# Kernel optimization log

Measured on AMD Instinct MI355X. Metric: run time of the kernel, lower is better.

## Reference

```python
import jax, jax.numpy as jnp
import numpy as np

BS = 4
EMBED = 256
HEADS = 8
LEVELS = 4
POINTS = 4
HD = EMBED // HEADS  # 32
SHAPES = np.array([[96, 96], [48, 48], [24, 24], [12, 12]], dtype=np.int64)
LQ = int((SHAPES[:, 0] * SHAPES[:, 1]).sum())  # 12240


def _offset_bias():
    # faithful to MSDeformableAttention._reset_parameters grid init
    thetas = np.arange(HEADS, dtype=np.float32) * (2.0 * np.pi / HEADS)
    g = np.stack([np.cos(thetas), np.sin(thetas)], -1)
    g = g / np.abs(g).max(-1, keepdims=True)
    g = np.tile(g.reshape(HEADS, 1, 1, 2), (1, LEVELS, POINTS, 1))
    g = g * np.arange(1, POINTS + 1, dtype=np.float32).reshape(1, 1, -1, 1)
    return jnp.asarray(g.reshape(-1), dtype=jnp.float32)


def setup_inputs() -> dict:
    key = jax.random.key(0)
    ks = jax.random.split(key, 8)
    tp = HEADS * LEVELS * POINTS
    d = {}
    d["query"] = jax.random.normal(ks[0], (BS, LQ, EMBED), jnp.float32)
    d["reference_points"] = jax.random.uniform(ks[1], (BS, LQ, LEVELS, 2), jnp.float32)
    d["value"] = jax.random.normal(ks[2], (BS, LQ, EMBED), jnp.float32)
    d["value_spatial_shapes"] = SHAPES  # static numpy, int
    d["W_off"] = jax.random.normal(ks[3], (EMBED, tp * 2), jnp.float32) * 0.01
    d["b_off"] = _offset_bias()
    d["W_attn"] = jax.random.normal(ks[4], (EMBED, tp), jnp.float32) * 0.02
    d["b_attn"] = jnp.zeros((tp,), jnp.float32)
    d["W_val"] = jax.random.normal(ks[5], (EMBED, EMBED), jnp.float32) * (1.0 / np.sqrt(EMBED).astype(np.float32))
    d["b_val"] = jnp.zeros((EMBED,), jnp.float32)
    d["W_out"] = jax.random.normal(ks[6], (EMBED, EMBED), jnp.float32) * (1.0 / np.sqrt(EMBED).astype(np.float32))
    d["b_out"] = jnp.zeros((EMBED,), jnp.float32)
    return d


def _bilinear_sample(img, grid):
    # img: [B,H,W,C]; grid: [B,Q,P,2] in [-1,1] (x,y)
    # matches F.grid_sample(mode='bilinear', padding_mode='zeros', align_corners=False)
    B, H, W, C = img.shape
    gx = (grid[..., 0] + 1.0) * (W * 0.5) - 0.5
    gy = (grid[..., 1] + 1.0) * (H * 0.5) - 0.5
    x0 = jnp.floor(gx)
    y0 = jnp.floor(gy)
    wx = gx - x0
    wy = gy - y0
    x0i = x0.astype(jnp.int32)
    y0i = y0.astype(jnp.int32)
    x1i = x0i + 1
    y1i = y0i + 1
    flat = img.reshape(B, H * W, C)

    def corner(xi, yi, w):
        valid = (xi >= 0) & (xi < W) & (yi >= 0) & (yi < H)
        idx = jnp.clip(yi, 0, H - 1) * W + jnp.clip(xi, 0, W - 1)
        v = jnp.take_along_axis(flat, idx.reshape(B, -1, 1), axis=1)
        v = v.reshape(idx.shape + (C,))
        return v * (w * valid)[..., None]

    return (corner(x0i, y0i, (1.0 - wx) * (1.0 - wy))
            + corner(x1i, y0i, wx * (1.0 - wy))
            + corner(x0i, y1i, (1.0 - wx) * wy)
            + corner(x1i, y1i, wx * wy))


def reference(query, reference_points, value, value_spatial_shapes,
              W_off, b_off, W_attn, b_attn, W_val, b_val, W_out, b_out):
    shapes = np.asarray(value_spatial_shapes)  # static [L,2] (H,W)
    bs, Lq, _ = query.shape
    v = (value @ W_val + b_val).reshape(bs, -1, HEADS, HD)  # [bs,Lv,H,hd]
    off = (query @ W_off + b_off).reshape(bs, Lq, HEADS, LEVELS, POINTS, 2)
    aw = jax.nn.softmax((query @ W_attn + b_attn).reshape(bs, Lq, HEADS, LEVELS * POINTS), axis=-1)
    aw = aw.reshape(bs, Lq, HEADS, LEVELS, POINTS)
    # normalizer is (W,H) per level
    norm = jnp.asarray(shapes[:, ::-1].copy(), jnp.float32).reshape(1, 1, 1, LEVELS, 1, 2)
    loc = reference_points[:, :, None, :, None, :] + off / norm
    grids = 2.0 * loc - 1.0  # [bs,Lq,H,L,P,2]

    acc = jnp.zeros((bs * HEADS, Lq, HD), query.dtype)
    start = 0
    for lvl in range(LEVELS):
        h, w = int(shapes[lvl, 0]), int(shapes[lvl, 1])
        v_l = v[:, start:start + h * w].reshape(bs, h, w, HEADS, HD)
        v_l = v_l.transpose(0, 3, 1, 2, 4).reshape(bs * HEADS, h, w, HD)
        g_l = grids[:, :, :, lvl].transpose(0, 2, 1, 3, 4).reshape(bs * HEADS, Lq, POINTS, 2)
        s_l = _bilinear_sample(v_l, g_l)  # [bs*H, Lq, P, hd]
        w_l = aw[:, :, :, lvl].transpose(0, 2, 1, 3).reshape(bs * HEADS, Lq, POINTS)
        acc = acc + jnp.einsum('bqpc,bqp->bqc', s_l, w_l)
        start += h * w

    out = acc.reshape(bs, HEADS, Lq, HD).transpose(0, 2, 1, 3).reshape(bs, Lq, EMBED)
    return out @ W_out + b_out
```

## Files before the change

kernel.cpp:

```cpp
#include <hip/hip_runtime.h>
#include <hip/hip_bf16.h>

static constexpr int BS     = 4;
static constexpr int EMBED  = 256;
static constexpr int HEADS  = 8;
static constexpr int LEVELS = 4;
static constexpr int POINTS = 4;
static constexpr int HD     = 32;
static constexpr int LQ     = 12240;
static constexpr int NROW   = BS * LQ;
static constexpr int LVL_W[4]  = {96, 48, 24, 12};
static constexpr int LVL_H[4]  = {96, 48, 24, 12};
static constexpr int LVL_ST[4] = {0, 9216, 11520, 12096};

typedef __attribute__((ext_vector_type(8))) short short8;
typedef __attribute__((ext_vector_type(4))) float f32x4;
typedef __attribute__((ext_vector_type(2))) float f32x2;
typedef _Float16 h2 __attribute__((ext_vector_type(2)));

__device__ __forceinline__ unsigned short f2bf(float f) {
    unsigned int u = __float_as_uint(f);
    unsigned int r = (u + 0x7FFFu + ((u >> 16) & 1u)) >> 16;
    return (unsigned short)r;
}

__device__ __forceinline__ unsigned int pkh(float a, float b) {
    const unsigned int ua = __builtin_bit_cast(unsigned short, (_Float16)a);
    const unsigned int ub = __builtin_bit_cast(unsigned short, (_Float16)b);
    return ua | (ub << 16);
}

__device__ __forceinline__ float dot2(float acc, unsigned int v, unsigned int w) {
#if __has_builtin(__builtin_amdgcn_fdot2)
    return __builtin_amdgcn_fdot2(__builtin_bit_cast(h2, v),
                                  __builtin_bit_cast(h2, w), acc, false);
#else
    asm("v_dot2_f32_f16 %0, %1, %2, %0" : "+v"(acc) : "v"(v), "v"(w));
    return acc;
#endif
}

__global__ __launch_bounds__(256) void prep_weights(
    const float* __restrict__ W_off, const float* __restrict__ W_attn,
    const float* __restrict__ W_val, const float* __restrict__ W_out,
    unsigned short* __restrict__ WT_oa, unsigned short* __restrict__ WT_val,
    unsigned short* __restrict__ WT_out)
{
    const int gid = blockIdx.x * 256 + threadIdx.x;
    const int k = gid & 255;
    const int n = gid >> 8;
    if (n < 384) {
        const float v = (n < 256) ? W_off[k * 256 + n] : W_attn[k * 128 + (n - 256)];
        WT_oa[n * 256 + k] = f2bf(v);
    } else if (n < 640) {
        const int nn = n - 384;
        WT_val[nn * 256 + k] = f2bf(W_val[k * 256 + nn]);
    } else {
        const int nn = n - 640;
        WT_out[nn * 256 + k] = f2bf(W_out[k * 256 + nn]);
    }
}

__global__ __launch_bounds__(256, 5) void gemm_vo(
    const float* __restrict__ Aval, const float* __restrict__ Aqry,
    const unsigned short* __restrict__ Wval, const unsigned short* __restrict__ Woa,
    const float* __restrict__ bval, const float* __restrict__ boff,
    const float* __restrict__ battn,
    unsigned short* __restrict__ Vout, float* __restrict__ OAout)
{
    constexpr int NTW = 2;
    constexpr int NB  = 128;
    constexpr int K   = 256;
    __shared__ __align__(16) unsigned short As[64][40];
    __shared__ __align__(16) unsigned short Bs[NB][40];

    const int x    = blockIdx.x;
    const bool isV = (x < 2);
    const float* A = isV ? Aval : Aqry;
    const unsigned short* Wt = isV ? Wval : Woa;
    const int n0   = isV ? x * 128 : (x - 2) * 128;

    const int tid = threadIdx.x;
    const int m0 = blockIdx.y * 64;
    const int w  = tid >> 6;
    const int l  = tid & 63;
    const int lm = l & 15;
    const int lq = l >> 4;

    const int sr = tid >> 2;
    const int kg = (tid & 3) * 8;

    float4 pa0, pa1;
    short8 pb[NTW];

    auto gload = [&](int k0) {
        const float* ap = &A[(size_t)(m0 + sr) * K + k0 + kg];
        pa0 = *(const float4*)ap;
        pa1 = *(const float4*)(ap + 4);
        #pragma unroll
        for (int i = 0; i < NTW; ++i) {
            const int slot = tid + i * 256;
            const int n  = slot >> 2;
            const int kk = (slot & 3) * 8;
            pb[i] = *(const short8*)&Wt[(size_t)(n0 + n) * K + k0 + kk];
        }
    };

    f32x4 acc[4][NTW];
    #pragma unroll
    for (int rg = 0; rg < 4; ++rg)
        #pragma unroll
        for (int nt = 0; nt < NTW; ++nt)
            acc[rg][nt] = (f32x4){0.f, 0.f, 0.f, 0.f};

    gload(0);
    #pragma unroll 2
    for (int k0 = 0; k0 < K; k0 += 32) {
        uint4 pk;
        pk.x = (unsigned int)f2bf(pa0.x) | ((unsigned int)f2bf(pa0.y) << 16);
        pk.y = (unsigned int)f2bf(pa0.z) | ((unsigned int)f2bf(pa0.w) << 16);
        pk.z = (unsigned int)f2bf(pa1.x) | ((unsigned int)f2bf(pa1.y) << 16);
        pk.w = (unsigned int)f2bf(pa1.z) | ((unsigned int)f2bf(pa1.w) << 16);
        *(uint4*)&As[sr][kg] = pk;
        #pragma unroll
        for (int i = 0; i < NTW; ++i) {
            const int slot = tid + i * 256;
            const int n  = slot >> 2;
            const int kk = (slot & 3) * 8;
            *(short8*)&Bs[n][kk] = pb[i];
        }
        __syncthreads();

        if (k0 + 32 < K) gload(k0 + 32);

        short8 af[4];
        #pragma unroll
        for (int rg = 0; rg < 4; ++rg)
            af[rg] = *(const short8*)&As[rg * 16 + lm][lq * 8];
        #pragma unroll
        for (int nt = 0; nt < NTW; ++nt) {
            const short8 bf = *(const short8*)&Bs[(w * NTW + nt) * 16 + lm][lq * 8];
            #pragma unroll
            for (int rg = 0; rg < 4; ++rg)
                acc[rg][nt] = __builtin_amdgcn_mfma_f32_16x16x32_bf16(af[rg], bf, acc[rg][nt], 0, 0, 0);
        }
        __syncthreads();
    }

    #pragma unroll
    for (int nt = 0; nt < NTW; ++nt) {
        const int col = n0 + (w * NTW + nt) * 16 + lm;
        float b;
        if (isV) b = bval[col];
        else     b = (col < 256) ? boff[col] : battn[col - 256];
        #pragma unroll
        for (int rg = 0; rg < 4; ++rg)
            #pragma unroll
            for (int r = 0; r < 4; ++r) {
                const int row = m0 + rg * 16 + lq * 4 + r;
                const float v = acc[rg][nt][r] + b;
                if (isV) Vout[(size_t)row * 256 + col] =
                             __builtin_bit_cast(unsigned short, (_Float16)v);
                else     OAout[(size_t)row * 384 + col] = v;
            }
    }
}

template <int NTW, bool A_BF16, bool OUT_BF16>
__global__ __launch_bounds__(256, 5) void gemm_mfma(
    const void* __restrict__ Av, const unsigned short* __restrict__ Wt,
    const float* __restrict__ bias0, const float* __restrict__ bias1, int nsplit,
    void* __restrict__ Cv, int N)
{
    constexpr int NB = NTW * 64;
    constexpr int K  = 256;
    __shared__ __align__(16) unsigned short As[64][40];
    __shared__ __align__(16) unsigned short Bs[NB][40];

    const int tid = threadIdx.x;
    const int m0 = blockIdx.y * 64;
    const int n0 = blockIdx.x * NB;
    const int w  = tid >> 6;
    const int l  = tid & 63;
    const int lm = l & 15;
    const int lq = l >> 4;

    const int sr = tid >> 2;
    const int kg = (tid & 3) * 8;

    float4 pa0, pa1; short8 pa_bf;
    short8 pb[NTW];

    auto gload = [&](int k0) {
        if (A_BF16) {
            const unsigned short* A = (const unsigned short*)Av;
            pa_bf = *(const short8*)&A[(size_t)(m0 + sr) * K + k0 + kg];
        } else {
            const float* A = (const float*)Av;
            const float* ap = &A[(size_t)(m0 + sr) * K + k0 + kg];
            pa0 = *(const float4*)ap;
            pa1 = *(const float4*)(ap + 4);
        }
        #pragma unroll
        for (int i = 0; i < NTW; ++i) {
            const int slot = tid + i * 256;
            const int n  = slot >> 2;
            const int kk = (slot & 3) * 8;
            pb[i] = *(const short8*)&Wt[(size_t)(n0 + n) * K + k0 + kk];
        }
    };

    f32x4 acc[4][NTW];
    #pragma unroll
    for (int rg = 0; rg < 4; ++rg)
        #pragma unroll
        for (int nt = 0; nt < NTW; ++nt)
            acc[rg][nt] = (f32x4){0.f, 0.f, 0.f, 0.f};

    gload(0);
    #pragma unroll 2
    for (int k0 = 0; k0 < K; k0 += 32) {
        if (A_BF16) {
            *(short8*)&As[sr][kg] = pa_bf;
        } else {
            uint4 pk;
            pk.x = (unsigned int)f2bf(pa0.x) | ((unsigned int)f2bf(pa0.y) << 16);
            pk.y = (unsigned int)f2bf(pa0.z) | ((unsigned int)f2bf(pa0.w) << 16);
            pk.z = (unsigned int)f2bf(pa1.x) | ((unsigned int)f2bf(pa1.y) << 16);
            pk.w = (unsigned int)f2bf(pa1.z) | ((unsigned int)f2bf(pa1.w) << 16);
            *(uint4*)&As[sr][kg] = pk;
        }
        #pragma unroll
        for (int i = 0; i < NTW; ++i) {
            const int slot = tid + i * 256;
            const int n  = slot >> 2;
            const int kk = (slot & 3) * 8;
            *(short8*)&Bs[n][kk] = pb[i];
        }
        __syncthreads();

        if (k0 + 32 < K) gload(k0 + 32);

        short8 af[4];
        #pragma unroll
        for (int rg = 0; rg < 4; ++rg)
            af[rg] = *(const short8*)&As[rg * 16 + lm][lq * 8];
        #pragma unroll
        for (int nt = 0; nt < NTW; ++nt) {
            const short8 bf = *(const short8*)&Bs[(w * NTW + nt) * 16 + lm][lq * 8];
            #pragma unroll
            for (int rg = 0; rg < 4; ++rg)
                acc[rg][nt] = __builtin_amdgcn_mfma_f32_16x16x32_bf16(af[rg], bf, acc[rg][nt], 0, 0, 0);
        }
        __syncthreads();
    }

    #pragma unroll
    for (int nt = 0; nt < NTW; ++nt) {
        const int col = n0 + (w * NTW + nt) * 16 + lm;
        const float b = (col < nsplit) ? bias0[col] : bias1[col - nsplit];
        #pragma unroll
        for (int rg = 0; rg < 4; ++rg)
            #pragma unroll
            for (int r = 0; r < 4; ++r) {
                const int row = m0 + rg * 16 + lq * 4 + r;
                const float v = acc[rg][nt][r] + b;
                if (OUT_BF16) ((unsigned short*)Cv)[(size_t)row * N + col] = f2bf(v);
                else          ((float*)Cv)[(size_t)row * N + col] = v;
            }
    }
}

__global__ __launch_bounds__(256, 7) void sample_kernel(
    const unsigned short* __restrict__ V,
    const float* __restrict__ OA,
    const float* __restrict__ refp,
    unsigned short* __restrict__ ACC)
{
    __shared__ __align__(16) unsigned int pr_o[512][4];
    __shared__ __align__(16) unsigned int pr_w[512][2];

    const int tid = threadIdx.x;

    const unsigned bx = blockIdx.x;
    const int xcd  = bx & 7;
    const int slot = bx >> 3;
    const int batch = xcd >> 1;
    const int wb   = slot * 2 + (xcd & 1);
    const int row0 = batch * LQ + wb * 4;

    {
        const int g = tid & 31;
        const int r = g >> 3;
        const int h = g & 7;
        const int L = tid >> 5;
        const int prow = row0 + r;
        const float* rowp = OA + (size_t)prow * 384;

        const float lg0 = rowp[256 + h * 16 + L];
        const float lg1 = rowp[256 + h * 16 + L + 8];

        float* smax = (float*)pr_w;
        float* ssum = smax + 264;
        smax[L * 33 + g] = fmaxf(lg0, lg1);
        __syncthreads();
        float m = smax[g];
        #pragma unroll
        for (int k = 1; k < 8; ++k) m = fmaxf(m, smax[k * 33 + g]);
        const float e0 = __expf(lg0 - m);
        const float e1 = __expf(lg1 - m);
        ssum[L * 33 + g] = e0 + e1;
        __syncthreads();
        float sden = ssum[g];
        #pragma unroll
        for (int k = 1; k < 8; ++k) sden += ssum[k * 33 + g];
        const float inv = 1.0f / sden;

        uint2 wstash[2];
        int   sidx[2];
        #pragma unroll
        for (int ss = 0; ss < 2; ++ss) {
            const int lp  = L + ss * 8;
            const int s   = lp * 32 + g;
            const int lvl = lp >> 2;
            const int Wl = LVL_W[lvl], Hl = LVL_H[lvl], st = LVL_ST[lvl];

            const float2 oxy = *(const float2*)&rowp[h * 32 + lp * 2];
            const float2 rxy = *(const float2*)&refp[(size_t)prow * 8 + lvl * 2];
            const float wgt = (ss ? e1 : e0) * inv;

            const float gx = (rxy.x + oxy.x / (float)Wl) * (float)Wl - 0.5f;
            const float gy = (rxy.y + oxy.y / (float)Hl) * (float)Hl - 0.5f;

            const float fx = floorf(gx), fy = floorf(gy);
            const float wx = gx - fx,    wy = gy - fy;
            const int x0 = (int)fx, y0 = (int)fy;
            const int x1 = x0 + 1,  y1 = y0 + 1;

            const bool bx0 = ((unsigned)x0 < (unsigned)Wl);
            const bool bx1 = ((unsigned)x1 < (unsigned)Wl);
            const bool by0 = ((unsigned)y0 < (unsigned)Hl);
            const bool by1 = ((unsigned)y1 < (unsigned)Hl);
            const float w00 = (bx0 && by0) ? (1.f - wx) * (1.f - wy) * wgt : 0.f;
            const float w10 = (bx1 && by0) ? wx * (1.f - wy) * wgt : 0.f;
            const float w01 = (bx0 && by1) ? (1.f - wx) * wy * wgt : 0.f;
            const float w11 = (bx1 && by1) ? wx * wy * wgt : 0.f;

            const int cx0 = min(max(x0, 0), Wl - 1);
            const int cx1 = min(max(x1, 0), Wl - 1);
            const int cy0 = min(max(y0, 0), Hl - 1);
            const int cy1 = min(max(y1, 0), Hl - 1);

            uint4 o;
            o.x = (unsigned int)(st + cy0 * Wl + cx0) * 512u;
            o.y = (unsigned int)(st + cy0 * Wl + cx1) * 512u;
            o.z = (unsigned int)(st + cy1 * Wl + cx0) * 512u;
            o.w = (unsigned int)(st + cy1 * Wl + cx1) * 512u;
            *(uint4*)&pr_o[s][0] = o;

            wstash[ss] = make_uint2(pkh(w00, w10), pkh(w01, w11));
            sidx[ss] = s;
        }
        __syncthreads();
        *(uint2*)&pr_w[sidx[0]][0] = wstash[0];
        *(uint2*)&pr_w[sidx[1]][0] = wstash[1];
    }
    __syncthreads();

    const int w    = tid >> 6;
    const int l    = tid & 63;
    const int half = l >> 5;
    const int head = (l >> 2) & 7;
    const int c16  = (l & 3) * 16;

    const int row  = __builtin_amdgcn_readfirstlane(row0 + w);
    const char* vrow = (const char*)V + (size_t)batch * ((size_t)LQ * 512);
    const unsigned int lane_byte = (unsigned int)(head * 64 + c16);
    const int sid0 = half * 256 + w * 8 + head;

    constexpr unsigned SEL_LO = 0x01000504u;
    constexpr unsigned SEL_HI = 0x03020706u;

    uint4 ofs[2];
    uint2 wpk[2];
    uint4 dat[2][4];
    float acc[8];
    #pragma unroll
    for (int i = 0; i < 8; ++i) acc[i] = 0.f;

    auto ldglb = [&](int buf) {
        const uint4 o = ofs[buf];
        dat[buf][0] = *(const uint4*)(vrow + (lane_byte + o.x));
        dat[buf][1] = *(const uint4*)(vrow + (lane_byte + o.y));
        dat[buf][2] = *(const uint4*)(vrow + (lane_byte + o.z));
        dat[buf][3] = *(const uint4*)(vrow + (lane_byte + o.w));
    };
    auto ldpr = [&](int j, int buf) {
        ofs[buf] = *(const uint4*)&pr_o[sid0 + j * 32][0];
        wpk[buf] = *(const uint2*)&pr_w[sid0 + j * 32][0];
    };
    auto cpair = [&](const uint4& d0, const uint4& d1, unsigned wp) {
        acc[0] = dot2(acc[0], __builtin_amdgcn_perm(d0.x, d1.x, SEL_LO), wp);
        acc[1] = dot2(acc[1], __builtin_amdgcn_perm(d0.x, d1.x, SEL_HI), wp);
        acc[2] = dot2(acc[2], __builtin_amdgcn_perm(d0.y, d1.y, SEL_LO), wp);
        acc[3] = dot2(acc[3], __builtin_amdgcn_perm(d0.y, d1.y, SEL_HI), wp);
        acc[4] = dot2(acc[4], __builtin_amdgcn_perm(d0.z, d1.z, SEL_LO), wp);
        acc[5] = dot2(acc[5], __builtin_amdgcn_perm(d0.z, d1.z, SEL_HI), wp);
        acc[6] = dot2(acc[6], __builtin_amdgcn_perm(d0.w, d1.w, SEL_LO), wp);
        acc[7] = dot2(acc[7], __builtin_amdgcn_perm(d0.w, d1.w, SEL_HI), wp);
    };
    auto consume = [&](int buf) {
        cpair(dat[buf][0], dat[buf][1], wpk[buf].x);
        cpair(dat[buf][2], dat[buf][3], wpk[buf].y);
    };

    ldpr(0, 0);
    ldpr(1, 1);
    ldglb(0);
    #pragma unroll
    for (int j = 0; j < 8; ++j) {
        if (j + 1 < 8) ldglb((j + 1) & 1);
        consume(j & 1);
        if (j + 2 < 8) ldpr(j + 2, j & 1);
    }

    #pragma unroll
    for (int i = 0; i < 8; ++i) acc[i] += __shfl_xor(acc[i], 32);

    if (half == 0) {
        uint4 o;
        o.x = (unsigned int)f2bf(acc[0]) | ((unsigned int)f2bf(acc[1]) << 16);
        o.y = (unsigned int)f2bf(acc[2]) | ((unsigned int)f2bf(acc[3]) << 16);
        o.z = (unsigned int)f2bf(acc[4]) | ((unsigned int)f2bf(acc[5]) << 16);
        o.w = (unsigned int)f2bf(acc[6]) | ((unsigned int)f2bf(acc[7]) << 16);
        *(uint4*)((char*)(ACC + (size_t)row * EMBED) + head * 64 + c16) = o;
    }
}

extern "C" void kernel_launch(void* const* d_in, const int* in_sizes, int n_in,
                              void* d_out, int out_size, void* d_ws, size_t ws_size,
                              hipStream_t stream) {
    const float* query  = (const float*)d_in[0];
    const float* refp   = (const float*)d_in[1];
    const float* value  = (const float*)d_in[2];
    const float* W_off  = (const float*)d_in[4];
    const float* b_off  = (const float*)d_in[5];
    const float* W_attn = (const float*)d_in[6];
    const float* b_attn = (const float*)d_in[7];
    const float* W_val  = (const float*)d_in[8];
    const float* b_val  = (const float*)d_in[9];
    const float* W_out  = (const float*)d_in[10];
    const float* b_out  = (const float*)d_in[11];
    float* out = (float*)d_out;

    unsigned short* WT_oa  = (unsigned short*)d_ws;
    unsigned short* WT_val = WT_oa  + 384 * 256;
    unsigned short* WT_out = WT_val + 256 * 256;
    unsigned short* V      = WT_out + 256 * 256;
    float*          OA     = (float*)(V + (size_t)NROW * EMBED);
    unsigned short* ACCb   = (unsigned short*)(OA + (size_t)NROW * 384);

    dim3 blk(256);

    prep_weights<<<896, blk, 0, stream>>>(W_off, W_attn, W_val, W_out,
                                          WT_oa, WT_val, WT_out);
    gemm_vo<<<dim3(5, NROW / 64), blk, 0, stream>>>(
        value, query, WT_val, WT_oa, b_val, b_off, b_attn, V, OA);
    sample_kernel<<<NROW / 4, blk, 0, stream>>>(V, OA, refp, ACCb);
    gemm_mfma<2, true, false><<<dim3(2, NROW / 64), blk, 0, stream>>>(
        ACCb, WT_out, b_out, b_out, 256, out, 256);
}
```

Baseline: 341.0 us.

## Use row-persistent GEMMs with full A tile in LDS and deepen sampler pipeline

Replaces the N-split GEMMs with a kernel where each block owns a 64-row strip, converts the whole A strip to bf16 once into LDS, and loops over 128-column chunks, so activations are read from global memory and converted only once. The fused value/offset GEMM is split into two launches. The sampler now stages the OA rows into LDS with a swizzled layout instead of reading them directly from global memory, and deepens its gather prefetch to three data buffers. This adds a larger LDS footprint and lower occupancy bounds, and the extra launch adds its own overhead.

```diff
diff --git a/kernel.cpp b/kernel.cpp
--- a/kernel.cpp
+++ b/kernel.cpp
@@ -15,7 +15,6 @@
 
 typedef __attribute__((ext_vector_type(8))) short short8;
 typedef __attribute__((ext_vector_type(4))) float f32x4;
-typedef __attribute__((ext_vector_type(2))) float f32x2;
 typedef _Float16 h2 __attribute__((ext_vector_type(2)));
 
 __device__ __forceinline__ unsigned short f2bf(float f) {
@@ -61,27 +60,18 @@
     }
 }
 
-__global__ __launch_bounds__(256, 5) void gemm_vo(
-    const float* __restrict__ Aval, const float* __restrict__ Aqry,
-    const unsigned short* __restrict__ Wval, const unsigned short* __restrict__ Woa,
-    const float* __restrict__ bval, const float* __restrict__ boff,
-    const float* __restrict__ battn,
-    unsigned short* __restrict__ Vout, float* __restrict__ OAout)
+template <int NCH, bool A_BF16, int OMODE>
+__global__ __launch_bounds__(256, 3) void gemm_persist(
+    const void* __restrict__ Av, const unsigned short* __restrict__ Wt,
+    const float* __restrict__ bias0, const float* __restrict__ bias1, int nsplit,
+    void* __restrict__ Cv)
 {
-    constexpr int NTW = 2;
-    constexpr int NB  = 128;
-    constexpr int K   = 256;
-    __shared__ __align__(16) unsigned short As[64][40];
-    __shared__ __align__(16) unsigned short Bs[NB][40];
-
-    const int x    = blockIdx.x;
-    const bool isV = (x < 2);
-    const float* A = isV ? Aval : Aqry;
-    const unsigned short* Wt = isV ? Wval : Woa;
-    const int n0   = isV ? x * 128 : (x - 2) * 128;
+    constexpr int K = 256;
+    __shared__ __align__(16) unsigned short Af[64][264];
+    __shared__ __align__(16) unsigned short Bs[128][40];
 
     const int tid = threadIdx.x;
-    const int m0 = blockIdx.y * 64;
+    const int m0 = blockIdx.x * 64;
     const int w  = tid >> 6;
     const int l  = tid & 63;
     const int lm = l & 15;
@@ -90,188 +80,101 @@
     const int sr = tid >> 2;
     const int kg = (tid & 3) * 8;
 
-    float4 pa0, pa1;
-    short8 pb[NTW];
-
-    auto gload = [&](int k0) {
-        const float* ap = &A[(size_t)(m0 + sr) * K + k0 + kg];
-        pa0 = *(const float4*)ap;
-        pa1 = *(const float4*)(ap + 4);
-        #pragma unroll
-        for (int i = 0; i < NTW; ++i) {
+    if (A_BF16) {
+        const unsigned short* A = (const unsigned short*)Av;
+        #pragma unroll
+        for (int k0 = 0; k0 < K; k0 += 32)
+            *(short8*)&Af[sr][k0 + kg] = *(const short8*)&A[(size_t)(m0 + sr) * K + k0 + kg];
+    } else {
+        const float* A = (const float*)Av;
+        #pragma unroll
+        for (int k0 = 0; k0 < K; k0 += 32) {
+            const float* ap = &A[(size_t)(m0 + sr) * K + k0 + kg];
+            const float4 a0 = *(const float4*)ap;
+            const float4 a1 = *(const float4*)(ap + 4);
+            uint4 pk;
+            pk.x = (unsigned int)f2bf(a0.x) | ((unsigned int)f2bf(a0.y) << 16);
+            pk.y = (unsigned int)f2bf(a0.z) | ((unsigned int)f2bf(a0.w) << 16);
+            pk.z = (unsigned int)f2bf(a1.x) | ((unsigned int)f2bf(a1.y) << 16);
+            pk.w = (unsigned int)f2bf(a1.z) | ((unsigned int)f2bf(a1.w) << 16);
+            *(uint4*)&Af[sr][k0 + kg] = pk;
+        }
+    }
+
+    short8 pb[2];
+    auto gloadB = [&](int n0, int k0) {
+        #pragma unroll
+        for (int i = 0; i < 2; ++i) {
             const int slot = tid + i * 256;
             const int n  = slot >> 2;
             const int kk = (slot & 3) * 8;
             pb[i] = *(const short8*)&Wt[(size_t)(n0 + n) * K + k0 + kk];
         }
     };
-
-    f32x4 acc[4][NTW];
+    gloadB(0, 0);
+    __syncthreads();
+
     #pragma unroll
-    for (int rg = 0; rg < 4; ++rg)
-        #pragma unroll
-        for (int nt = 0; nt < NTW; ++nt)
-            acc[rg][nt] = (f32x4){0.f, 0.f, 0.f, 0.f};
-
-    gload(0);
-    #pragma unroll 2
-    for (int k0 = 0; k0 < K; k0 += 32) {
-        uint4 pk;
-        pk.x = (unsigned int)f2bf(pa0.x) | ((unsigned int)f2bf(pa0.y) << 16);
-        pk.y = (unsigned int)f2bf(pa0.z) | ((unsigned int)f2bf(pa0.w) << 16);
-        pk.z = (unsigned int)f2bf(pa1.x) | ((unsigned int)f2bf(pa1.y) << 16);
-        pk.w = (unsigned int)f2bf(pa1.z) | ((unsigned int)f2bf(pa1.w) << 16);
-        *(uint4*)&As[sr][kg] = pk;
-        #pragma unroll
-        for (int i = 0; i < NTW; ++i) {
-            const int slot = tid + i * 256;
-            const int n  = slot >> 2;
-            const int kk = (slot & 3) * 8;
-            *(short8*)&Bs[n][kk] = pb[i];
-        }
-        __syncthreads();
-
-        if (k0 + 32 < K) gload(k0 + 32);
-
-        short8 af[4];
-        #pragma unroll
-        for (int rg = 0; rg < 4; ++rg)
-            af[rg] = *(const short8*)&As[rg * 16 + lm][lq * 8];
-        #pragma unroll
-        for (int nt = 0; nt < NTW; ++nt) {
-            const short8 bf = *(const short8*)&Bs[(w * NTW + nt) * 16 + lm][lq * 8];
+    for (int ch = 0; ch < NCH; ++ch) {
+        const int n0 = ch * 128;
+        f32x4 acc[4][2];
+        #pragma unroll
+        for (int rg = 0; rg < 4; ++rg) {
+            acc[rg][0] = (f32x4){0.f, 0.f, 0.f, 0.f};
+            acc[rg][1] = (f32x4){0.f, 0.f, 0.f, 0.f};
+        }
+
+        #pragma unroll 2
+        for (int k0 = 0; k0 < K; k0 += 32) {
+            #pragma unroll
+            for (int i = 0; i < 2; ++i) {
+                const int slot = tid + i * 256;
+                const int n  = slot >> 2;
+                const int kk = (slot & 3) * 8;
+                *(short8*)&Bs[n][kk] = pb[i];
+            }
+            __syncthreads();
+
+            if (k0 + 32 < K)       gloadB(n0, k0 + 32);
+            else if (ch + 1 < NCH) gloadB(n0 + 128, 0);
+
+            short8 af[4];
             #pragma unroll
             for (int rg = 0; rg < 4; ++rg)
-                acc[rg][nt] = __builtin_amdgcn_mfma_f32_16x16x32_bf16(af[rg], bf, acc[rg][nt], 0, 0, 0);
-        }
-        __syncthreads();
-    }
-
-    #pragma unroll
-    for (int nt = 0; nt < NTW; ++nt) {
-        const int col = n0 + (w * NTW + nt) * 16 + lm;
-        float b;
-        if (isV) b = bval[col];
-        else     b = (col < 256) ? boff[col] : battn[col - 256];
-        #pragma unroll
-        for (int rg = 0; rg < 4; ++rg)
+                af[rg] = *(const short8*)&Af[rg * 16 + lm][k0 + lq * 8];
             #pragma unroll
-            for (int r = 0; r < 4; ++r) {
-                const int row = m0 + rg * 16 + lq * 4 + r;
-                const float v = acc[rg][nt][r] + b;
-                if (isV) Vout[(size_t)row * 256 + col] =
-                             __builtin_bit_cast(unsigned short, (_Float16)v);
-                else     OAout[(size_t)row * 384 + col] = v;
+            for (int nt = 0; nt < 2; ++nt) {
+                const short8 bf = *(const short8*)&Bs[(w * 2 + nt) * 16 + lm][lq * 8];
+                #pragma unroll
+                for (int rg = 0; rg < 4; ++rg)
+                    acc[rg][nt] = __builtin_amdgcn_mfma_f32_16x16x32_bf16(af[rg], bf, acc[rg][nt], 0, 0, 0);
             }
-    }
-}
-
-template <int NTW, bool A_BF16, bool OUT_BF16>
-__global__ __launch_bounds__(256, 5) void gemm_mfma(
-    const void* __restrict__ Av, const unsigned short* __restrict__ Wt,
-    const float* __restrict__ bias0, const float* __restrict__ bias1, int nsplit,
-    void* __restrict__ Cv, int N)
-{
-    constexpr int NB = NTW * 64;
-    constexpr int K  = 256;
-    __shared__ __align__(16) unsigned short As[64][40];
-    __shared__ __align__(16) unsigned short Bs[NB][40];
-
-    const int tid = threadIdx.x;
-    const int m0 = blockIdx.y * 64;
-    const int n0 = blockIdx.x * NB;
-    const int w  = tid >> 6;
-    const int l  = tid & 63;
-    const int lm = l & 15;
-    const int lq = l >> 4;
-
-    const int sr = tid >> 2;
-    const int kg = (tid & 3) * 8;
-
-    float4 pa0, pa1; short8 pa_bf;
-    short8 pb[NTW];
-
-    auto gload = [&](int k0) {
-        if (A_BF16) {
-            const unsigned short* A = (const unsigned short*)Av;
-            pa_bf = *(const short8*)&A[(size_t)(m0 + sr) * K + k0 + kg];
-        } else {
-            const float* A = (const float*)Av;
-            const float* ap = &A[(size_t)(m0 + sr) * K + k0 + kg];
-            pa0 = *(const float4*)ap;
-            pa1 = *(const float4*)(ap + 4);
-        }
-        #pragma unroll
-        for (int i = 0; i < NTW; ++i) {
-            const int slot = tid + i * 256;
-            const int n  = slot >> 2;
-            const int kk = (slot & 3) * 8;
-            pb[i] = *(const short8*)&Wt[(size_t)(n0 + n) * K + k0 + kk];
-        }
-    };
-
-    f32x4 acc[4][NTW];
-    #pragma unroll
-    for (int rg = 0; rg < 4; ++rg)
-        #pragma unroll
-        for (int nt = 0; nt < NTW; ++nt)
-            acc[rg][nt] = (f32x4){0.f, 0.f, 0.f, 0.f};
-
-    gload(0);
-    #pragma unroll 2
-    for (int k0 = 0; k0 < K; k0 += 32) {
-        if (A_BF16) {
-            *(short8*)&As[sr][kg] = pa_bf;
-        } else {
-            uint4 pk;
-            pk.x = (unsigned int)f2bf(pa0.x) | ((unsigned int)f2bf(pa0.y) << 16);
-            pk.y = (unsigned int)f2bf(pa0.z) | ((unsigned int)f2bf(pa0.w) << 16);
-            pk.z = (unsigned int)f2bf(pa1.x) | ((unsigned int)f2bf(pa1.y) << 16);
-            pk.w = (unsigned int)f2bf(pa1.z) | ((unsigned int)f2bf(pa1.w) << 16);
-            *(uint4*)&As[sr][kg] = pk;
-        }
-        #pragma unroll
-        for (int i = 0; i < NTW; ++i) {
-            const int slot = tid + i * 256;
-            const int n  = slot >> 2;
-            const int kk = (slot & 3) * 8;
-            *(short8*)&Bs[n][kk] = pb[i];
-        }
-        __syncthreads();
-
-        if (k0 + 32 < K) gload(k0 + 32);
-
-        short8 af[4];
-        #pragma unroll
-        for (int rg = 0; rg < 4; ++rg)
-            af[rg] = *(const short8*)&As[rg * 16 + lm][lq * 8];
-        #pragma unroll
-        for (int nt = 0; nt < NTW; ++nt) {
-            const short8 bf = *(const short8*)&Bs[(w * NTW + nt) * 16 + lm][lq * 8];
+            __syncthreads();
+        }
+
+        #pragma unroll
+        for (int nt = 0; nt < 2; ++nt) {
+            const int col = n0 + (w * 2 + nt) * 16 + lm;
+            const float b = (col < nsplit) ? bias0[col] : bias1[col - nsplit];
             #pragma unroll
             for (int rg = 0; rg < 4; ++rg)
-                acc[rg][nt] = __builtin_amdgcn_mfma_f32_16x16x32_bf16(af[rg], bf, acc[rg][nt], 0, 0, 0);
-        }
-        __syncthreads();
-    }
-
-    #pragma unroll
-    for (int nt = 0; nt < NTW; ++nt) {
-        const int col = n0 + (w * NTW + nt) * 16 + lm;
-        const float b = (col < nsplit) ? bias0[col] : bias1[col - nsplit];
-        #pragma unroll
-        for (int rg = 0; rg < 4; ++rg)
-            #pragma unroll
-            for (int r = 0; r < 4; ++r) {
-                const int row = m0 + rg * 16 + lq * 4 + r;
-                const float v = acc[rg][nt][r] + b;
-                if (OUT_BF16) ((unsigned short*)Cv)[(size_t)row * N + col] = f2bf(v);
-                else          ((float*)Cv)[(size_t)row * N + col] = v;
-            }
-    }
-}
-
-__global__ __launch_bounds__(256, 7) void sample_kernel(
+                #pragma unroll
+                for (int r = 0; r < 4; ++r) {
+                    const int row = m0 + rg * 16 + lq * 4 + r;
+                    const float v = acc[rg][nt][r] + b;
+                    if (OMODE == 0)
+                        ((unsigned short*)Cv)[(size_t)row * 256 + col] =
+                            __builtin_bit_cast(unsigned short, (_Float16)v);
+                    else if (OMODE == 1)
+                        ((float*)Cv)[(size_t)row * 384 + col] = v;
+                    else
+                        ((float*)Cv)[(size_t)row * 256 + col] = v;
+                }
+        }
+    }
+}
+
+__global__ __launch_bounds__(256, 4) void sample_kernel(
     const unsigned short* __restrict__ V,
     const float* __restrict__ OA,
     const float* __restrict__ refp,
@@ -290,15 +193,30 @@
     const int row0 = batch * LQ + wb * 4;
 
     {
+        float4* dstb = (float4*)pr_o;
+        const float4* src = (const float4*)(OA + (size_t)row0 * 384);
+        {
+            const int i = tid, rr = i / 96, ww = i % 96;
+            dstb[rr * 96 + (ww ^ ((ww >> 3) & 7))] = src[i];
+        }
+        if (tid < 128) {
+            const int i = tid + 256, rr = i / 96, ww = i % 96;
+            dstb[rr * 96 + (ww ^ ((ww >> 3) & 7))] = src[i];
+        }
+        __syncthreads();
+
         const int g = tid & 31;
         const int r = g >> 3;
         const int h = g & 7;
         const int L = tid >> 5;
-        const int prow = row0 + r;
-        const float* rowp = OA + (size_t)prow * 384;
-
-        const float lg0 = rowp[256 + h * 16 + L];
-        const float lg1 = rowp[256 + h * 16 + L + 8];
+        const float* stg = (const float*)pr_o + r * 384;
+
+        auto swzf4 = [](int f4) { return f4 ^ ((f4 >> 3) & 7); };
+
+        const int f4l0 = 64 + ((h * 16 + L) >> 2);
+        const int f4l1 = 64 + ((h * 16 + L + 8) >> 2);
+        const float lg0 = stg[swzf4(f4l0) * 4 + (L & 3)];
+        const float lg1 = stg[swzf4(f4l1) * 4 + (L & 3)];
 
         float* smax = (float*)pr_w;
         float* ssum = smax + 264;
@@ -316,6 +234,7 @@
         for (int k = 1; k < 8; ++k) sden += ssum[k * 33 + g];
         const float inv = 1.0f / sden;
 
+        uint4 ostash[2];
         uint2 wstash[2];
         int   sidx[2];
         #pragma unroll
@@ -325,8 +244,9 @@
             const int lvl = lp >> 2;
             const int Wl = LVL_W[lvl], Hl = LVL_H[lvl], st = LVL_ST[lvl];
 
-            const float2 oxy = *(const float2*)&rowp[h * 32 + lp * 2];
-            const float2 rxy = *(const float2*)&refp[(size_t)prow * 8 + lvl * 2];
+            const int f4c = h * 8 + (lp >> 1);
+            const float2 oxy = *(const float2*)&stg[swzf4(f4c) * 4 + (lp & 1) * 2];
+            const float2 rxy = *(const float2*)&refp[(size_t)(row0 + r) * 8 + lvl * 2];
             const float wgt = (ss ? e1 : e0) * inv;
 
             const float gx = (rxy.x + oxy.x / (float)Wl) * (float)Wl - 0.5f;
@@ -356,12 +276,13 @@
             o.y = (unsigned int)(st + cy0 * Wl + cx1) * 512u;
             o.z = (unsigned int)(st + cy1 * Wl + cx0) * 512u;
             o.w = (unsigned int)(st + cy1 * Wl + cx1) * 512u;
-            *(uint4*)&pr_o[s][0] = o;
-
+            ostash[ss] = o;
             wstash[ss] = make_uint2(pkh(w00, w10), pkh(w01, w11));
             sidx[ss] = s;
         }
         __syncthreads();
+        *(uint4*)&pr_o[sidx[0]][0] = ostash[0];
+        *(uint4*)&pr_o[sidx[1]][0] = ostash[1];
         *(uint2*)&pr_w[sidx[0]][0] = wstash[0];
         *(uint2*)&pr_w[sidx[1]][0] = wstash[1];
     }
@@ -381,23 +302,23 @@
     constexpr unsigned SEL_LO = 0x01000504u;
     constexpr unsigned SEL_HI = 0x03020706u;
 
-    uint4 ofs[2];
-    uint2 wpk[2];
-    uint4 dat[2][4];
+    uint4 ofs[4];
+    uint2 wpk[4];
+    uint4 dat[3][4];
     float acc[8];
     #pragma unroll
     for (int i = 0; i < 8; ++i) acc[i] = 0.f;
 
-    auto ldglb = [&](int buf) {
-        const uint4 o = ofs[buf];
-        dat[buf][0] = *(const uint4*)(vrow + (lane_byte + o.x));
-        dat[buf][1] = *(const uint4*)(vrow + (lane_byte + o.y));
-        dat[buf][2] = *(const uint4*)(vrow + (lane_byte + o.z));
-        dat[buf][3] = *(const uint4*)(vrow + (lane_byte + o.w));
-    };
-    auto ldpr = [&](int j, int buf) {
-        ofs[buf] = *(const uint4*)&pr_o[sid0 + j * 32][0];
-        wpk[buf] = *(const uint2*)&pr_w[sid0 + j * 32][0];
+    auto ldpr = [&](int j, int sl) {
+        ofs[sl] = *(const uint4*)&pr_o[sid0 + j * 32][0];
+        wpk[sl] = *(const uint2*)&pr_w[sid0 + j * 32][0];
+    };
+    auto ldglb = [&](int osl, int dsl) {
+        const uint4 o = ofs[osl];
+        dat[dsl][0] = *(const uint4*)(vrow + (lane_byte + o.x));
+        dat[dsl][1] = *(const uint4*)(vrow + (lane_byte + o.y));
+        dat[dsl][2] = *(const uint4*)(vrow + (lane_byte + o.z));
+        dat[dsl][3] = *(const uint4*)(vrow + (lane_byte + o.w));
     };
     auto cpair = [&](const uint4& d0, const uint4& d1, unsigned wp) {
         acc[0] = dot2(acc[0], __builtin_amdgcn_perm(d0.x, d1.x, SEL_LO), wp);
@@ -409,19 +330,18 @@
         acc[6] = dot2(acc[6], __builtin_amdgcn_perm(d0.w, d1.w, SEL_LO), wp);
         acc[7] = dot2(acc[7], __builtin_amdgcn_perm(d0.w, d1.w, SEL_HI), wp);
     };
-    auto consume = [&](int buf) {
-        cpair(dat[buf][0], dat[buf][1], wpk[buf].x);
-        cpair(dat[buf][2], dat[buf][3], wpk[buf].y);
-    };
-
-    ldpr(0, 0);
-    ldpr(1, 1);
-    ldglb(0);
+    auto consume = [&](int dsl, int wsl) {
+        cpair(dat[dsl][0], dat[dsl][1], wpk[wsl].x);
+        cpair(dat[dsl][2], dat[dsl][3], wpk[wsl].y);
+    };
+
+    ldpr(0, 0); ldpr(1, 1); ldpr(2, 2);
+    ldglb(0, 0); ldglb(1, 1);
     #pragma unroll
     for (int j = 0; j < 8; ++j) {
-        if (j + 1 < 8) ldglb((j + 1) & 1);
-        consume(j & 1);
-        if (j + 2 < 8) ldpr(j + 2, j & 1);
+        if (j + 2 < 8) ldglb((j + 2) & 3, (j + 2) % 3);
+        if (j + 3 < 8) ldpr(j + 3, (j + 3) & 3);
+        consume(j % 3, j & 3);
     }
 
     #pragma unroll
@@ -464,9 +384,11 @@
 
     prep_weights<<<896, blk, 0, stream>>>(W_off, W_attn, W_val, W_out,
                                           WT_oa, WT_val, WT_out);
-    gemm_vo<<<dim3(5, NROW / 64), blk, 0, stream>>>(
-        value, query, WT_val, WT_oa, b_val, b_off, b_attn, V, OA);
+    gemm_persist<2, false, 0><<<NROW / 64, blk, 0, stream>>>(
+        value, WT_val, b_val, b_val, 256, V);
+    gemm_persist<3, false, 1><<<NROW / 64, blk, 0, stream>>>(
+        query, WT_oa, b_off, b_attn, 256, OA);
     sample_kernel<<<NROW / 4, blk, 0, stream>>>(V, OA, refp, ACCb);
-    gemm_mfma<2, true, false><<<dim3(2, NROW / 64), blk, 0, stream>>>(
-        ACCb, WT_out, b_out, b_out, 256, out, 256);
-}
+    gemm_persist<2, true, 2><<<NROW / 64, blk, 0, stream>>>(
+        ACCb, WT_out, b_out, b_out, 256, out);
+}
```

New measurement: 320.1 us. 6.1% less time.
